# Kernel optimization log

Measured on AMD Instinct MI355X. Metric: run time of the kernel, lower is better.

## Reference

```python
import jax, jax.numpy as jnp
import numpy as np

M = 32768   # query points
N = 10000   # gaussians
F = 32      # features per gaussian
K = 16      # neighbors
EPS = 1e-8


def setup_inputs() -> dict:
    key = jax.random.key(0)
    k1, k2, k3, k4 = jax.random.split(key, 4)
    coords = jax.random.uniform(k1, (M, 3), dtype=jnp.float32)            # query points in [0,1]^3
    means = jax.random.uniform(k2, (N, 3), dtype=jnp.float32)             # gaussian centers
    # module init: log_covs = log(1e-4); add small noise to make grads non-degenerate
    log_covs = jnp.full((N, 3), np.log(1e-4), dtype=jnp.float32) \
        + 0.1 * jax.random.normal(k3, (N, 3), dtype=jnp.float32)
    feats = jax.random.normal(k4, (N, F), dtype=jnp.float32)              # hash-encoded per-gaussian features (buffer)
    return {"coords": coords, "means": means, "log_covs": log_covs, "feats": feats, "k": K}


def reference(coords, means, log_covs, feats, k):
    # --- brute-force KNN over gaussian means ---
    # d2: [M, N] squared distances
    d2 = jnp.sum((coords[:, None, :] - means[None, :, :]) ** 2, axis=-1)
    _, idx = jax.lax.top_k(-d2, k)                     # idx: [M, K] nearest gaussian indices

    # --- gather per-gaussian params ---
    mu = means[idx]                                    # [M, K, 3]
    cov = jnp.exp(log_covs)[idx]                       # [M, K, 3] diagonal covariances
    f = feats[idx]                                     # [M, K, F]

    # --- anisotropic gaussian kernel weights ---
    diff = coords[:, None, :] - mu                     # [M, K, 3]
    logw = -0.5 * jnp.sum(diff * diff / cov, axis=-1)  # [M, K]
    w = jnp.exp(logw)

    # --- normalized splash aggregation -> [M, F] ---
    out = jnp.einsum('mk,mkf->mf', w, f) / (jnp.sum(w, axis=-1, keepdims=True) + EPS)
    return out
```

## Files before the change

kernel.cpp:

```cpp
#include <hip/hip_runtime.h>


typedef short bf16x8 __attribute__((ext_vector_type(8)));
typedef float f32x4  __attribute__((ext_vector_type(4)));

constexpr int   M_Q   = 32768;
constexpr int   N_G   = 10000;
constexpr float EPS   = 1e-8f;
constexpr int   GD    = 10;
constexpr int   NCELL = GD * GD * GD;
constexpr int   MAXC  = 448;
constexpr int   KCH   = 64;
constexpr int   NPAD  = 10240;

#define W_GCNT   0
#define W_QCNT   1000
#define W_GSTART 2000
#define W_QSTART 3000
#define W_GCUR   4000
#define W_QCUR   5000
#define W_SORTQ  6000
#define W_SMI    38768
#define W_SCRD   118768
#define W_FGT    249840

__device__ __forceinline__ int cell_of(float x, float y, float z) {
    int cx = min(max((int)(x * (float)GD), 0), GD - 1);
    int cy = min(max((int)(y * (float)GD), 0), GD - 1);
    int cz = min(max((int)(z * (float)GD), 0), GD - 1);
    return (cx * GD + cy) * GD + cz;
}

__device__ __forceinline__ ushort f2bf(float x) {
    union { float f; unsigned u; } v; v.f = x;
    unsigned r = v.u + 0x7FFFu + ((v.u >> 16) & 1u);
    return (ushort)(r >> 16);
}

__global__ __launch_bounds__(256)
void k_count(const float* __restrict__ coords,
             const float* __restrict__ means,
             int* __restrict__ W)
{
    const int t = blockIdx.x * 256 + threadIdx.x;
    if (t < N_G)
        atomicAdd(W + W_GCNT + cell_of(means[t*3+0], means[t*3+1], means[t*3+2]), 1);
    if (t < M_Q)
        atomicAdd(W + W_QCNT + cell_of(coords[t*3+0], coords[t*3+1], coords[t*3+2]), 1);
}

__global__ __launch_bounds__(256)
void k_scan(int* __restrict__ W)
{
    __shared__ int wp[4];
    const int bid = blockIdx.x, tid = threadIdx.x;
    const int* cnt = W + (bid ? W_QCNT   : W_GCNT);
    int*       st  = W + (bid ? W_QSTART : W_GSTART);
    int*       cu  = W + (bid ? W_QCUR   : W_GCUR);
    const int lane = tid & 63, wid = tid >> 6;
    int carry = 0;
    for (int base = 0; base < 1024; base += 256) {
        const int idx = base + tid;
        int v = (idx < NCELL) ? cnt[idx] : 0;
        int x = v;
        #pragma unroll
        for (int o = 1; o < 64; o <<= 1) { int y = __shfl_up(x, o); if (lane >= o) x += y; }
        if (lane == 63) wp[wid] = x;
        __syncthreads();
        int off = carry, tot = 0;
        #pragma unroll
        for (int k = 0; k < 4; ++k) { tot += wp[k]; if (k < wid) off += wp[k]; }
        if (idx < NCELL) { int ex = off + x - v; st[idx] = ex; cu[idx] = ex; }
        carry += tot;
        __syncthreads();
    }
}

__global__ __launch_bounds__(256)
void k_scatter(const float* __restrict__ coords,
               const float* __restrict__ means,
               const float* __restrict__ log_covs,
               const float* __restrict__ feats,
               int* __restrict__ W)
{
    const int t = blockIdx.x * 256 + threadIdx.x;
    if (t < N_G) {
        const int c = cell_of(means[t*3+0], means[t*3+1], means[t*3+2]);
        const int slot = atomicAdd(W + W_GCUR + c, 1);
        float4* smi = (float4*)(W + W_SMI);
        float4 m; m.x = means[t*3+0]; m.y = means[t*3+1]; m.z = means[t*3+2]; m.w = 0.f;
        float4 a; a.x = 0.5f * __expf(-log_covs[t*3+0]);
                  a.y = 0.5f * __expf(-log_covs[t*3+1]);
                  a.z = 0.5f * __expf(-log_covs[t*3+2]); a.w = 0.f;
        smi[2*slot]   = m;
        smi[2*slot+1] = a;
        ushort* fgt = (ushort*)(W + W_FGT);
        const float4* f4 = (const float4*)feats;
        #pragma unroll
        for (int k = 0; k < 8; ++k) {
            float4 v = f4[t*8 + k];
            fgt[(k*4+0)*NPAD + slot] = f2bf(v.x);
            fgt[(k*4+1)*NPAD + slot] = f2bf(v.y);
            fgt[(k*4+2)*NPAD + slot] = f2bf(v.z);
            fgt[(k*4+3)*NPAD + slot] = f2bf(v.w);
        }
    }
    if (t < M_Q) {
        const int c = cell_of(coords[t*3+0], coords[t*3+1], coords[t*3+2]);
        const int slot = atomicAdd(W + W_QCUR + c, 1);
        W[W_SORTQ + slot] = t;
        float4 q; q.x = coords[t*3+0]; q.y = coords[t*3+1]; q.z = coords[t*3+2]; q.w = 0.f;
        ((float4*)(W + W_SCRD))[slot] = q;
    }
}

__global__ __launch_bounds__(256, 4)
void k_splash(const int* __restrict__ W, float* __restrict__ out)
{
    __shared__ int    ldsIdx[MAXC];
    __shared__ float4 ldsQ[64];
    __shared__ int    qList[64];
    __shared__ ushort Wq[64][72];
    __shared__ ushort Ft[32][72];
    __shared__ float  ldsWS[64];

    const int cell = blockIdx.x;
    const int tid  = threadIdx.x, lane = tid & 63, wv = tid >> 6;

    const int qStart = W[W_QSTART + cell];
    const int qCnt   = W[W_QCNT   + cell];
    if (qCnt == 0) return;

    const int cx = cell / 100, cyy = (cell / 10) % 10, cz = cell % 10;
    const int z0 = max(cz - 1, 0), z1 = min(cz + 1, GD - 1);
    int sStart[9], sOff[9];
    int T = 0;
    #pragma unroll
    for (int k = 0; k < 9; ++k) {
        const int ax = cx + k / 3 - 1, ay = cyy + k % 3 - 1;
        const bool ok = ((unsigned)ax < (unsigned)GD) && ((unsigned)ay < (unsigned)GD);
        const int cb = (ax * GD + ay) * GD;
        const int jb = ok ? W[W_GSTART + cb + z0] : 0;
        const int je = ok ? (W[W_GSTART + cb + z1] + W[W_GCNT + cb + z1]) : 0;
        sStart[k] = jb; sOff[k] = T;
        T += (je > jb) ? (je - jb) : 0;
    }
    if (T > MAXC) T = MAXC;

    for (int i = tid; i < T; i += 256) {
        int s = 0;
        #pragma unroll
        for (int k = 0; k < 9; ++k) {
            const int hi = (k == 8) ? T : sOff[k + 1];
            if (i >= sOff[k] && i < hi) s = sStart[k] + (i - sOff[k]);
        }
        ldsIdx[i] = s;
    }

    const float4* smi4  = (const float4*)(W + W_SMI);
    const float4* scrd4 = (const float4*)(W + W_SCRD);
    const ushort* fgt   = (const ushort*)(W + W_FGT);

    const int nkch = (T + KCH - 1) / KCH;

    for (int qb = 0; qb < qCnt; qb += 64) {
        const int qw = min(qCnt - qb, 64);
        __syncthreads();
        if (tid < 64) {
            const int qi = min(tid, qw - 1);
            ldsQ[tid]  = scrd4[qStart + qb + qi];
            qList[tid] = W[W_SORTQ + qStart + qb + qi];
        }
        __syncthreads();

        f32x4 acc0 = {0,0,0,0}, acc1 = {0,0,0,0}, acc2 = {0,0,0,0};
        const bool waveActive = (wv * 16) < qw;
        const short ov = ((lane & 15) == 0) ? (short)0x3F80 : (short)0;
        const bf16x8 bones = {ov,ov,ov,ov,ov,ov,ov,ov};

        for (int c = 0; c < nkch; ++c) {
            const int cb = c * KCH;
            const int  fi  = cb + lane;
            const bool kOK = fi < T;
            const int  s   = kOK ? ldsIdx[fi] : 0;
            const float4 gm = smi4[2*s];
            const float4 ga = smi4[2*s+1];
            #pragma unroll
            for (int r = 0; r < 8; ++r) {
                const int v = tid + r * 256;
                const int f = v >> 6, kc = v & 63;
                const int f2 = cb + kc;
                Ft[f][kc] = (f2 < T) ? fgt[f * NPAD + ldsIdx[f2]] : (ushort)0;
            }
            __syncthreads();

            if (waveActive) {
                #pragma unroll
                for (int qq = 0; qq < 16; ++qq) {
                    const int q = wv * 16 + qq;
                    const float4 qv = ldsQ[q];
                    const float dx = qv.x - gm.x, dy = qv.y - gm.y, dz = qv.z - gm.z;
                    const float s2 = dx*dx*ga.x + dy*dy*ga.y + dz*dz*ga.z;
                    const float w  = kOK ? __expf(-s2) : 0.f;
                    Wq[q][lane] = f2bf(w);
                }
            }
            __syncthreads();

            if (waveActive) {
                #pragma unroll
                for (int ks = 0; ks < 2; ++ks) {
                    const int k0 = ks * 32 + ((lane >> 4) << 3);
                    const bf16x8 a  = *(const bf16x8*)&Wq[wv*16 + (lane & 15)][k0];
                    const bf16x8 b0 = *(const bf16x8*)&Ft[(lane & 15)][k0];
                    const bf16x8 b1 = *(const bf16x8*)&Ft[16 + (lane & 15)][k0];
                    acc0 = __builtin_amdgcn_mfma_f32_16x16x32_bf16(a, b0,    acc0, 0, 0, 0);
                    acc1 = __builtin_amdgcn_mfma_f32_16x16x32_bf16(a, b1,    acc1, 0, 0, 0);
                    acc2 = __builtin_amdgcn_mfma_f32_16x16x32_bf16(a, bones, acc2, 0, 0, 0);
                }
            }
            __syncthreads();
        }

        if (waveActive && (lane & 15) == 0) {
            #pragma unroll
            for (int i = 0; i < 4; ++i)
                ldsWS[wv*16 + ((lane >> 4) << 2) + i] = acc2[i];
        }
        __syncthreads();

        if (waveActive) {
            const int fl = lane & 15;
            #pragma unroll
            for (int i = 0; i < 4; ++i) {
                const int q = wv*16 + ((lane >> 4) << 2) + i;
                if (q < qw) {
                    const float inv = 1.0f / (ldsWS[q] + EPS);
                    const int qo = qList[q];
                    out[qo*32 + fl]      = acc0[i] * inv;
                    out[qo*32 + 16 + fl] = acc1[i] * inv;
                }
            }
        }
    }
}

extern "C" void kernel_launch(void* const* d_in, const int* in_sizes, int n_in,
                              void* d_out, int out_size, void* d_ws, size_t ws_size,
                              hipStream_t stream)
{
    const float* coords   = (const float*)d_in[0];
    const float* means    = (const float*)d_in[1];
    const float* log_covs = (const float*)d_in[2];
    const float* feats    = (const float*)d_in[3];
    float* out            = (float*)d_out;
    int*   W              = (int*)d_ws;

    hipMemsetAsync(W, 0, 2000 * sizeof(int), stream);

    hipLaunchKernelGGL(k_count,   dim3(128),   dim3(256), 0, stream, coords, means, W);
    hipLaunchKernelGGL(k_scan,    dim3(2),     dim3(256), 0, stream, W);
    hipLaunchKernelGGL(k_scatter, dim3(128),   dim3(256), 0, stream, coords, means, log_covs, feats, W);
    hipLaunchKernelGGL(k_splash,  dim3(NCELL), dim3(256), 0, stream, W, out);
}
```

Measured before the change: 107.1 us.

## Fuse prep kernels via cooperative launch and stage all features in LDS once

The memset, count, scan and scatter launches are merged into one cooperative kernel that uses grid-wide syncs, with the old multi-kernel path kept as a fallback if the cooperative launch fails. In the splash kernel, the bf16 features of all candidate gaussians (now capped at 384 instead of 448) are loaded into LDS once per cell rather than once per chunk per query batch. This removes the per-chunk block barriers, and the weight-sum normalizer is read with a wave shuffle instead of going through LDS. The aim is to cut launch overhead and repeated feature gathers. The cost is a larger LDS footprint that may lower occupancy, the grid-sync overhead, and a lower candidate cap that could drop neighbours in dense cells.

Result: slower. 167.1 us (+56.0%).

```diff
diff --git a/kernel.cpp b/kernel.cpp
--- a/kernel.cpp
+++ b/kernel.cpp
@@ -1,4 +1,7 @@
 #include <hip/hip_runtime.h>
+#include <hip/hip_cooperative_groups.h>
+
+namespace cg = cooperative_groups;
 
 
 typedef short bf16x8 __attribute__((ext_vector_type(8)));
@@ -9,8 +12,8 @@
 constexpr float EPS   = 1e-8f;
 constexpr int   GD    = 10;
 constexpr int   NCELL = GD * GD * GD;
-constexpr int   MAXC  = 448;
-constexpr int   KCH   = 64;
+constexpr int   MAXC  = 384;
+constexpr int   FTP   = 392;
 constexpr int   NPAD  = 10240;
 
 #define W_GCNT   0
@@ -37,92 +40,117 @@
     return (ushort)(r >> 16);
 }
 
-__global__ __launch_bounds__(256)
-void k_count(const float* __restrict__ coords,
-             const float* __restrict__ means,
-             int* __restrict__ W)
-{
-    const int t = blockIdx.x * 256 + threadIdx.x;
-    if (t < N_G)
-        atomicAdd(W + W_GCNT + cell_of(means[t*3+0], means[t*3+1], means[t*3+2]), 1);
-    if (t < M_Q)
-        atomicAdd(W + W_QCNT + cell_of(coords[t*3+0], coords[t*3+1], coords[t*3+2]), 1);
-}
-
-__global__ __launch_bounds__(256)
-void k_scan(int* __restrict__ W)
-{
-    __shared__ int wp[4];
-    const int bid = blockIdx.x, tid = threadIdx.x;
-    const int* cnt = W + (bid ? W_QCNT   : W_GCNT);
-    int*       st  = W + (bid ? W_QSTART : W_GSTART);
-    int*       cu  = W + (bid ? W_QCUR   : W_GCUR);
-    const int lane = tid & 63, wid = tid >> 6;
-    int carry = 0;
-    for (int base = 0; base < 1024; base += 256) {
-        const int idx = base + tid;
-        int v = (idx < NCELL) ? cnt[idx] : 0;
-        int x = v;
-        #pragma unroll
-        for (int o = 1; o < 64; o <<= 1) { int y = __shfl_up(x, o); if (lane >= o) x += y; }
-        if (lane == 63) wp[wid] = x;
-        __syncthreads();
-        int off = carry, tot = 0;
-        #pragma unroll
-        for (int k = 0; k < 4; ++k) { tot += wp[k]; if (k < wid) off += wp[k]; }
-        if (idx < NCELL) { int ex = off + x - v; st[idx] = ex; cu[idx] = ex; }
-        carry += tot;
-        __syncthreads();
-    }
-}
-
-__global__ __launch_bounds__(256)
-void k_scatter(const float* __restrict__ coords,
-               const float* __restrict__ means,
-               const float* __restrict__ log_covs,
-               const float* __restrict__ feats,
-               int* __restrict__ W)
-{
-    const int t = blockIdx.x * 256 + threadIdx.x;
-    if (t < N_G) {
-        const int c = cell_of(means[t*3+0], means[t*3+1], means[t*3+2]);
+
+__device__ __forceinline__ void phase_count(int gid,
+                                            const float* __restrict__ coords,
+                                            const float* __restrict__ means,
+                                            int* __restrict__ W) {
+    if (gid < N_G)
+        atomicAdd(W + W_GCNT + cell_of(means[gid*3+0], means[gid*3+1], means[gid*3+2]), 1);
+    if (gid < M_Q)
+        atomicAdd(W + W_QCNT + cell_of(coords[gid*3+0], coords[gid*3+1], coords[gid*3+2]), 1);
+}
+
+__device__ __forceinline__ void phase_scan(int bid, int tid, int* wp,
+                                           int* __restrict__ W) {
+    if (bid < 2) {
+        const int* cnt = W + (bid ? W_QCNT   : W_GCNT);
+        int*       st  = W + (bid ? W_QSTART : W_GSTART);
+        int*       cu  = W + (bid ? W_QCUR   : W_GCUR);
+        const int lane = tid & 63, wid = tid >> 6;
+        int carry = 0;
+        for (int base = 0; base < 1024; base += 256) {
+            const int idx = base + tid;
+            int v = (idx < NCELL) ? cnt[idx] : 0;
+            int x = v;
+            #pragma unroll
+            for (int o = 1; o < 64; o <<= 1) { int y = __shfl_up(x, o); if (lane >= o) x += y; }
+            if (lane == 63) wp[wid] = x;
+            __syncthreads();
+            int off = carry, tot = 0;
+            #pragma unroll
+            for (int k = 0; k < 4; ++k) { tot += wp[k]; if (k < wid) off += wp[k]; }
+            if (idx < NCELL) { int ex = off + x - v; st[idx] = ex; cu[idx] = ex; }
+            carry += tot;
+            __syncthreads();
+        }
+    }
+}
+
+__device__ __forceinline__ void phase_scatter(int gid,
+                                              const float* __restrict__ coords,
+                                              const float* __restrict__ means,
+                                              const float* __restrict__ log_covs,
+                                              const float* __restrict__ feats,
+                                              int* __restrict__ W) {
+    if (gid < N_G) {
+        const int c = cell_of(means[gid*3+0], means[gid*3+1], means[gid*3+2]);
         const int slot = atomicAdd(W + W_GCUR + c, 1);
         float4* smi = (float4*)(W + W_SMI);
-        float4 m; m.x = means[t*3+0]; m.y = means[t*3+1]; m.z = means[t*3+2]; m.w = 0.f;
-        float4 a; a.x = 0.5f * __expf(-log_covs[t*3+0]);
-                  a.y = 0.5f * __expf(-log_covs[t*3+1]);
-                  a.z = 0.5f * __expf(-log_covs[t*3+2]); a.w = 0.f;
+        float4 m; m.x = means[gid*3+0]; m.y = means[gid*3+1]; m.z = means[gid*3+2]; m.w = 0.f;
+        float4 a; a.x = 0.5f * __expf(-log_covs[gid*3+0]);
+                  a.y = 0.5f * __expf(-log_covs[gid*3+1]);
+                  a.z = 0.5f * __expf(-log_covs[gid*3+2]); a.w = 0.f;
         smi[2*slot]   = m;
         smi[2*slot+1] = a;
         ushort* fgt = (ushort*)(W + W_FGT);
         const float4* f4 = (const float4*)feats;
         #pragma unroll
         for (int k = 0; k < 8; ++k) {
-            float4 v = f4[t*8 + k];
+            float4 v = f4[gid*8 + k];
             fgt[(k*4+0)*NPAD + slot] = f2bf(v.x);
             fgt[(k*4+1)*NPAD + slot] = f2bf(v.y);
             fgt[(k*4+2)*NPAD + slot] = f2bf(v.z);
             fgt[(k*4+3)*NPAD + slot] = f2bf(v.w);
         }
     }
-    if (t < M_Q) {
-        const int c = cell_of(coords[t*3+0], coords[t*3+1], coords[t*3+2]);
+    if (gid < M_Q) {
+        const int c = cell_of(coords[gid*3+0], coords[gid*3+1], coords[gid*3+2]);
         const int slot = atomicAdd(W + W_QCUR + c, 1);
-        W[W_SORTQ + slot] = t;
-        float4 q; q.x = coords[t*3+0]; q.y = coords[t*3+1]; q.z = coords[t*3+2]; q.w = 0.f;
+        W[W_SORTQ + slot] = gid;
+        float4 q; q.x = coords[gid*3+0]; q.y = coords[gid*3+1]; q.z = coords[gid*3+2]; q.w = 0.f;
         ((float4*)(W + W_SCRD))[slot] = q;
     }
+}
+
+__global__ __launch_bounds__(256, 4)
+void k_prep(const float* __restrict__ coords, const float* __restrict__ means,
+            const float* __restrict__ log_covs, const float* __restrict__ feats,
+            int* __restrict__ W)
+{
+    __shared__ int wp[4];
+    cg::grid_group g = cg::this_grid();
+    const int tid = threadIdx.x, bid = blockIdx.x, gid = bid * 256 + tid;
+
+    if (gid < 2000) W[W_GCNT + gid] = 0;
+    g.sync();
+    phase_count(gid, coords, means, W);
+    g.sync();
+    phase_scan(bid, tid, wp, W);
+    g.sync();
+    phase_scatter(gid, coords, means, log_covs, feats, W);
+}
+
+__global__ __launch_bounds__(256) void k_count(const float* c, const float* m, int* W) {
+    phase_count(blockIdx.x * 256 + threadIdx.x, c, m, W);
+}
+__global__ __launch_bounds__(256) void k_scan(int* W) {
+    __shared__ int wp[4];
+    phase_scan(blockIdx.x, threadIdx.x, wp, W);
+}
+__global__ __launch_bounds__(256) void k_scatter(const float* c, const float* m,
+                                                 const float* lc, const float* f, int* W) {
+    phase_scatter(blockIdx.x * 256 + threadIdx.x, c, m, lc, f, W);
 }
 
 __global__ __launch_bounds__(256, 4)
 void k_splash(const int* __restrict__ W, float* __restrict__ out)
 {
     __shared__ int    ldsIdx[MAXC];
+    __shared__ ushort FtT[32][FTP];
     __shared__ float4 ldsQ[64];
     __shared__ int    qList[64];
     __shared__ ushort Wq[64][72];
-    __shared__ ushort Ft[32][72];
-    __shared__ float  ldsWS[64];
 
     const int cell = blockIdx.x;
     const int tid  = threadIdx.x, lane = tid & 63, wv = tid >> 6;
@@ -156,12 +184,25 @@
         }
         ldsIdx[i] = s;
     }
+    __syncthreads();
 
     const float4* smi4  = (const float4*)(W + W_SMI);
     const float4* scrd4 = (const float4*)(W + W_SCRD);
     const ushort* fgt   = (const ushort*)(W + W_FGT);
 
-    const int nkch = (T + KCH - 1) / KCH;
+    {
+        const int ia = tid, ib = tid + 256;
+        const int idA = (ia < T) ? ldsIdx[ia] : -1;
+        const int idB = (ib < T) ? ldsIdx[ib] : -1;
+        #pragma unroll 8
+        for (int f = 0; f < 32; ++f) {
+            FtT[f][ia] = (idA >= 0) ? fgt[f * NPAD + idA] : (ushort)0;
+            if (ib < MAXC)
+                FtT[f][ib] = (idB >= 0) ? fgt[f * NPAD + idB] : (ushort)0;
+        }
+    }
+
+    const int nkch = (T + 63) >> 6;
 
     for (int qb = 0; qb < qCnt; qb += 64) {
         const int qw = min(qCnt - qb, 64);
@@ -173,69 +214,47 @@
         }
         __syncthreads();
 
+        const bool waveActive = (wv * 16) < qw;
         f32x4 acc0 = {0,0,0,0}, acc1 = {0,0,0,0}, acc2 = {0,0,0,0};
-        const bool waveActive = (wv * 16) < qw;
         const short ov = ((lane & 15) == 0) ? (short)0x3F80 : (short)0;
         const bf16x8 bones = {ov,ov,ov,ov,ov,ov,ov,ov};
 
-        for (int c = 0; c < nkch; ++c) {
-            const int cb = c * KCH;
-            const int  fi  = cb + lane;
-            const bool kOK = fi < T;
-            const int  s   = kOK ? ldsIdx[fi] : 0;
-            const float4 gm = smi4[2*s];
-            const float4 ga = smi4[2*s+1];
-            #pragma unroll
-            for (int r = 0; r < 8; ++r) {
-                const int v = tid + r * 256;
-                const int f = v >> 6, kc = v & 63;
-                const int f2 = cb + kc;
-                Ft[f][kc] = (f2 < T) ? fgt[f * NPAD + ldsIdx[f2]] : (ushort)0;
-            }
-            __syncthreads();
-
-            if (waveActive) {
+        if (waveActive) {
+            for (int c = 0; c < nkch; ++c) {
+                const int cb = c << 6;
+                const int fi = cb + lane;
+                const bool kOK = fi < T;
+                const int  s   = kOK ? ldsIdx[fi] : 0;
+                const float4 gm = smi4[2*s];
+                const float4 ga = smi4[2*s+1];
                 #pragma unroll
                 for (int qq = 0; qq < 16; ++qq) {
-                    const int q = wv * 16 + qq;
+                    const int q = wv*16 + qq;
                     const float4 qv = ldsQ[q];
                     const float dx = qv.x - gm.x, dy = qv.y - gm.y, dz = qv.z - gm.z;
                     const float s2 = dx*dx*ga.x + dy*dy*ga.y + dz*dz*ga.z;
                     const float w  = kOK ? __expf(-s2) : 0.f;
                     Wq[q][lane] = f2bf(w);
                 }
-            }
-            __syncthreads();
-
-            if (waveActive) {
                 #pragma unroll
                 for (int ks = 0; ks < 2; ++ks) {
-                    const int k0 = ks * 32 + ((lane >> 4) << 3);
+                    const int k0 = (ks << 5) + ((lane >> 4) << 3);
                     const bf16x8 a  = *(const bf16x8*)&Wq[wv*16 + (lane & 15)][k0];
-                    const bf16x8 b0 = *(const bf16x8*)&Ft[(lane & 15)][k0];
-                    const bf16x8 b1 = *(const bf16x8*)&Ft[16 + (lane & 15)][k0];
+                    const bf16x8 b0 = *(const bf16x8*)&FtT[(lane & 15)][cb + k0];
+                    const bf16x8 b1 = *(const bf16x8*)&FtT[16 + (lane & 15)][cb + k0];
                     acc0 = __builtin_amdgcn_mfma_f32_16x16x32_bf16(a, b0,    acc0, 0, 0, 0);
                     acc1 = __builtin_amdgcn_mfma_f32_16x16x32_bf16(a, b1,    acc1, 0, 0, 0);
                     acc2 = __builtin_amdgcn_mfma_f32_16x16x32_bf16(a, bones, acc2, 0, 0, 0);
                 }
             }
-            __syncthreads();
-        }
-
-        if (waveActive && (lane & 15) == 0) {
-            #pragma unroll
-            for (int i = 0; i < 4; ++i)
-                ldsWS[wv*16 + ((lane >> 4) << 2) + i] = acc2[i];
-        }
-        __syncthreads();
-
-        if (waveActive) {
+
             const int fl = lane & 15;
             #pragma unroll
             for (int i = 0; i < 4; ++i) {
+                const float ws = __shfl(acc2[i], lane & 48);
                 const int q = wv*16 + ((lane >> 4) << 2) + i;
                 if (q < qw) {
-                    const float inv = 1.0f / (ldsWS[q] + EPS);
+                    const float inv = 1.0f / (ws + EPS);
                     const int qo = qList[q];
                     out[qo*32 + fl]      = acc0[i] * inv;
                     out[qo*32 + 16 + fl] = acc1[i] * inv;
@@ -256,10 +275,16 @@
     float* out            = (float*)d_out;
     int*   W              = (int*)d_ws;
 
-    hipMemsetAsync(W, 0, 2000 * sizeof(int), stream);
-
-    hipLaunchKernelGGL(k_count,   dim3(128),   dim3(256), 0, stream, coords, means, W);
-    hipLaunchKernelGGL(k_scan,    dim3(2),     dim3(256), 0, stream, W);
-    hipLaunchKernelGGL(k_scatter, dim3(128),   dim3(256), 0, stream, coords, means, log_covs, feats, W);
-    hipLaunchKernelGGL(k_splash,  dim3(NCELL), dim3(256), 0, stream, W, out);
-}
+    void* args[] = { (void*)&coords, (void*)&means, (void*)&log_covs,
+                     (void*)&feats,  (void*)&W };
+    hipError_t e = hipLaunchCooperativeKernel((const void*)k_prep,
+                                              dim3(128), dim3(256),
+                                              args, 0, stream);
+    if (e != hipSuccess) {
+        hipMemsetAsync(W, 0, 2000 * sizeof(int), stream);
+        hipLaunchKernelGGL(k_count,   dim3(128), dim3(256), 0, stream, coords, means, W);
+        hipLaunchKernelGGL(k_scan,    dim3(2),   dim3(256), 0, stream, W);
+        hipLaunchKernelGGL(k_scatter, dim3(128), dim3(256), 0, stream, coords, means, log_covs, feats, W);
+    }
+    hipLaunchKernelGGL(k_splash, dim3(NCELL), dim3(256), 0, stream, W, out);
+}
```
